# Optimization experiments

Hardware: AMD Instinct MI355X
Metric: run time of the kernel (lower is better)

The kernel has to match this reference:

```python
import jax, jax.numpy as jnp
import numpy as np

DIM, HEADS, B, S = 128, 4, 8, 80
BN_SCALE = np.float32(1.0 / np.sqrt(1.0 + 1e-5))  # eval-mode BatchNorm2d with running stats (0, 1)


def conv2d(x, w, b=None, groups=1, pad=0):
    y = jax.lax.conv_general_dilated(x, w, (1, 1), [(pad, pad), (pad, pad)],
                                     dimension_numbers=('NCHW', 'OIHW', 'NCHW'),
                                     feature_group_count=groups)
    return y if b is None else y + b[None, :, None, None]


def gate(x, w1, b1, g, bt, w2, b2):
    # Conv1x1 -> BatchNorm2d(eval) -> ReLU -> Conv1x1 -> Sigmoid
    y = conv2d(x, w1, b1)
    y = y * (g * BN_SCALE)[None, :, None, None] + bt[None, :, None, None]
    return jax.nn.sigmoid(conv2d(jax.nn.relu(y), w2, b2))


def layernorm(x, w, b):
    # Restormer WithBias LayerNorm over the channel dim
    mu = jnp.mean(x, 1, keepdims=True)
    var = jnp.var(x, 1, keepdims=True)
    return (x - mu) / jnp.sqrt(var + 1e-5) * w[None, :, None, None] + b[None, :, None, None]


def l2norm(x):
    # F.normalize(dim=-1) incl. complex: divide by L2 norm of |x|
    n = jnp.sqrt(jnp.sum(jnp.abs(x) ** 2, -1, keepdims=True))
    return x / jnp.maximum(n, 1e-12)


def split_heads(t):
    b, c, h, w = t.shape
    return t.reshape(b, HEADS, c // HEADS, h * w)


def _etb(x, ln1_w, ln1_b, ln2_w, ln2_b,
         f_temp, f_proj_w, f_w1, f_wb1, f_bn_g, f_bn_b, f_w2, f_wb2,
         s_temp, s_q1_w, s_q1_b, s_k1_w, s_k1_b, s_v1_w, s_v1_b,
         s_q3_w, s_q5_w, s_k3_w, s_k5_w, s_v3_w, s_v5_w, s_c3_w, s_c5_w, s_proj_w,
         ff_dw1_w, ff_dw2_w, ff_proj_w,
         ffg_w1, ffg_b1, ffg_bng, ffg_bnb, ffg_w2, ffg_b2,
         ffg1_w1, ffg1_b1, ffg1_bng, ffg1_bnb, ffg1_w2, ffg1_b2):
    b, c, h, w = x.shape
    G = c // 2
    xn = layernorm(x, ln1_w, ln1_b)
    # ---- Attention_F (the repeated fft2(x) calls in torch are identical; computed once) ----
    xf = jnp.fft.fft2(xn)
    qf = l2norm(split_heads(xf))  # q_f == k_f in the original code
    vf = split_heads(xf)
    attn = jnp.einsum('bhcn,bhdn->bhcd', qf, qf) * f_temp
    attn = jax.nn.softmax(attn.real, -1) + 1j * jax.nn.softmax(attn.imag, -1)
    # NOTE: torch applies ifft2 over the LAST TWO dims of [b, head, c, h*w] -> (c, h*w)
    out_f = jnp.abs(jnp.fft.ifft2(jnp.einsum('bhcd,bhdn->bhcn', attn, vf))).reshape(b, c, h, w)
    out_f_l = jnp.abs(jnp.fft.ifft2(gate(xf.real, f_w1, f_wb1, f_bn_g, f_bn_b, f_w2, f_wb2) * xf))
    a_f = conv2d(jnp.concatenate([out_f, out_f_l], 1), f_proj_w)
    # ---- Attention_S ----
    q1 = conv2d(xn, s_q1_w, s_q1_b)
    k1 = conv2d(xn, s_k1_w, s_k1_b)
    v1 = conv2d(xn, s_v1_w, s_v1_b)
    qs = jnp.concatenate([conv2d(q1, s_q3_w, groups=G, pad=1), conv2d(q1, s_q5_w, groups=G, pad=2)], 1)
    ks = jnp.concatenate([conv2d(k1, s_k3_w, groups=G, pad=1), conv2d(k1, s_k5_w, groups=G, pad=2)], 1)
    vs = jnp.concatenate([conv2d(v1, s_v3_w, groups=G, pad=1), conv2d(v1, s_v5_w, groups=G, pad=2)], 1)
    qn = l2norm(split_heads(qs))
    kn = l2norm(split_heads(ks))
    vh = split_heads(vs)
    attn_s = jax.nn.softmax(jnp.einsum('bhcn,bhdn->bhcd', qn, kn) * s_temp, -1)
    out_s = jnp.einsum('bhcd,bhdn->bhcn', attn_s, vh).reshape(b, c, h, w)
    out_s_l = jnp.concatenate([conv2d(xn, s_c3_w, groups=G, pad=1), conv2d(xn, s_c5_w, groups=G, pad=2)], 1)
    a_s = conv2d(jnp.concatenate([out_s, out_s_l], 1), s_proj_w)
    x = x + a_f + a_s
    # ---- FeedForward ----
    xn2 = layernorm(x, ln2_w, ln2_b)
    xf2 = jnp.fft.fft2(xn2)
    x_f = jnp.abs(gate(xf2.real, ffg_w1, ffg_b1, ffg_bng, ffg_bnb, ffg_w2, ffg_b2) * xf2)
    x_f_g = jax.nn.gelu(x_f, approximate=False) * x_f
    x_s = conv2d(xn2, ff_dw1_w, groups=c, pad=1)
    x_s_g = jax.nn.gelu(x_s, approximate=False) * x_s
    cat = jnp.concatenate([x_f_g, x_s_g], 1)  # [b, 2c, h, w]
    cf = jnp.fft.fft2(cat)
    x_f2b = jnp.abs(jnp.fft.ifft2(gate(cf.real, ffg1_w1, ffg1_b1, ffg1_bng, ffg1_bnb, ffg1_w2, ffg1_b2) * cf))
    x_s2b = conv2d(cat, ff_dw2_w, groups=c, pad=1)
    return x + conv2d(jnp.concatenate([x_f2b, x_s2b], 1), ff_proj_w)


def setup_inputs() -> dict:
    key = jax.random.key(0)
    ks = iter(jax.random.split(key, 64))
    rn = lambda shape, s=0.02: jax.random.normal(next(ks), shape, jnp.float32) * s
    d = {}
    d['x'] = jax.random.normal(next(ks), (B, DIM, S, S), jnp.float32)
    for n in ('ln1_w', 'ln2_w'):
        d[n] = jnp.ones((DIM,), jnp.float32)
    for n in ('ln1_b', 'ln2_b'):
        d[n] = jnp.zeros((DIM,), jnp.float32)
    d['f_temp'] = jnp.ones((HEADS, 1, 1), jnp.float32)
    d['s_temp'] = jnp.ones((HEADS, 1, 1), jnp.float32)
    d['f_proj_w'] = rn((DIM, 2 * DIM, 1, 1))
    d['s_proj_w'] = rn((DIM, 2 * DIM, 1, 1))
    r = DIM // 16
    d['f_w1'] = rn((r, DIM, 1, 1)); d['f_wb1'] = jnp.zeros((r,), jnp.float32)
    d['f_bn_g'] = jnp.ones((r,), jnp.float32); d['f_bn_b'] = jnp.zeros((r,), jnp.float32)
    d['f_w2'] = rn((DIM, r, 1, 1)); d['f_wb2'] = jnp.zeros((DIM,), jnp.float32)
    for n in ('s_q1', 's_k1', 's_v1'):
        d[n + '_w'] = rn((DIM, DIM, 1, 1)); d[n + '_b'] = jnp.zeros((DIM,), jnp.float32)
    for n in ('s_q3', 's_k3', 's_v3', 's_c3'):
        d[n + '_w'] = rn((DIM // 2, 2, 3, 3))
    for n in ('s_q5', 's_k5', 's_v5', 's_c5'):
        d[n + '_w'] = rn((DIM // 2, 2, 5, 5))
    d['ff_dw1_w'] = rn((DIM, 1, 3, 3))
    d['ff_dw2_w'] = rn((2 * DIM, 2, 3, 3))
    d['ff_proj_w'] = rn((DIM, 4 * DIM, 1, 1))
    d['ffg_w1'] = rn((r, DIM, 1, 1)); d['ffg_b1'] = jnp.zeros((r,), jnp.float32)
    d['ffg_bng'] = jnp.ones((r,), jnp.float32); d['ffg_bnb'] = jnp.zeros((r,), jnp.float32)
    d['ffg_w2'] = rn((DIM, r, 1, 1)); d['ffg_b2'] = jnp.zeros((DIM,), jnp.float32)
    d['ffg1_w1'] = rn((r, 2 * DIM, 1, 1)); d['ffg1_b1'] = jnp.zeros((r,), jnp.float32)
    d['ffg1_bng'] = jnp.ones((r,), jnp.float32); d['ffg1_bnb'] = jnp.zeros((r,), jnp.float32)
    d['ffg1_w2'] = rn((2 * DIM, r, 1, 1)); d['ffg1_b2'] = jnp.zeros((2 * DIM,), jnp.float32)
    return d


def reference(x, ln1_w, ln1_b, ln2_w, ln2_b,
              f_temp, f_proj_w, f_w1, f_wb1, f_bn_g, f_bn_b, f_w2, f_wb2,
              s_temp, s_q1_w, s_q1_b, s_k1_w, s_k1_b, s_v1_w, s_v1_b,
              s_q3_w, s_q5_w, s_k3_w, s_k5_w, s_v3_w, s_v5_w, s_c3_w, s_c5_w, s_proj_w,
              ff_dw1_w, ff_dw2_w, ff_proj_w,
              ffg_w1, ffg_b1, ffg_bng, ffg_bnb, ffg_w2, ffg_b2,
              ffg1_w1, ffg1_b1, ffg1_bng, ffg1_bnb, ffg1_w2, ffg1_b2):
    return _etb(x, ln1_w, ln1_b, ln2_w, ln2_b,
                f_temp, f_proj_w, f_w1, f_wb1, f_bn_g, f_bn_b, f_w2, f_wb2,
                s_temp, s_q1_w, s_q1_b, s_k1_w, s_k1_b, s_v1_w, s_v1_b,
                s_q3_w, s_q5_w, s_k3_w, s_k5_w, s_v3_w, s_v5_w, s_c3_w, s_c5_w, s_proj_w,
                ff_dw1_w, ff_dw2_w, ff_proj_w,
                ffg_w1, ffg_b1, ffg_bng, ffg_bnb, ffg_w2, ffg_b2,
                ffg1_w1, ffg1_b1, ffg1_bng, ffg1_bnb, ffg1_w2, ffg1_b2)
```

## Files before the change

kernel.cpp:

```cpp
#include <hip/hip_runtime.h>
#include <math.h>

#define DI __device__ __forceinline__

constexpr int B_ = 8, C_ = 128, H_ = 4, S_ = 80, N_ = 6400;
constexpr int P_ = B_ * N_;
constexpr int NSPL = 2;
constexpr float PI2 = 6.283185307179586f;
constexpr float BN_SC = 0.9999950000374997f;

typedef __attribute__((ext_vector_type(8))) short bf16x8;
typedef __attribute__((ext_vector_type(4))) float f32x4;

DI void cfma(float2& a, float2 u, float2 v) {
  a.x = fmaf(u.x, v.x, a.x); a.x = fmaf(-u.y, v.y, a.x);
  a.y = fmaf(u.x, v.y, a.y); a.y = fmaf(u.y, v.x, a.y);
}
DI float2 cmul(float2 u, float2 v) {
  return make_float2(u.x * v.x - u.y * v.y, u.x * v.y + u.y * v.x);
}
DI float gelu_mul(float m) {
  return 0.5f * m * (1.f + erff(m * 0.7071067811865476f)) * m;
}
DI unsigned short bf16_rn(float f) {
  union { float f; unsigned int u; } v; v.f = f;
  unsigned int u = v.u;
  return (unsigned short)((u + 0x7fffu + ((u >> 16) & 1u)) >> 16);
}

__global__ __launch_bounds__(256) void k_layernorm(const float* __restrict__ in,
    const float* __restrict__ w, const float* __restrict__ bb, float* __restrict__ out) {
  __shared__ float redS[4][64], redS2[4][64];
  __shared__ float muv[64], invv[64];
  const int tid = threadIdx.x;
  const int g = tid >> 6, l = tid & 63;
  const int p = blockIdx.x * 64 + l;
  const int b = p / N_, n = p % N_;
  const float* xp = in + (size_t)b * C_ * N_ + n;
  float s = 0.f, s2 = 0.f;
  for (int c = g * 32; c < g * 32 + 32; c++) {
    float v = xp[(size_t)c * N_];
    s += v; s2 = fmaf(v, v, s2);
  }
  redS[g][l] = s; redS2[g][l] = s2;
  __syncthreads();
  if (g == 0) {
    float ts  = redS[0][l] + redS[1][l] + redS[2][l] + redS[3][l];
    float ts2 = redS2[0][l] + redS2[1][l] + redS2[2][l] + redS2[3][l];
    float mu = ts * (1.f / C_);
    float var = ts2 * (1.f / C_) - mu * mu;
    muv[l] = mu; invv[l] = rsqrtf(var + 1e-5f);
  }
  __syncthreads();
  const float mu = muv[l], inv = invv[l];
  float* op = out + (size_t)b * C_ * N_ + n;
  for (int c = g * 32; c < g * 32 + 32; c++) {
    float v = xp[(size_t)c * N_];
    op[(size_t)c * N_] = (v - mu) * inv * w[c] + bb[c];
  }
}


__global__ __launch_bounds__(256) void k_fft2_r2c(const float* __restrict__ in, float2* __restrict__ out,
                                                  int nCh, int inCtot, int inCoff,
                                                  float2* __restrict__ out2, int inCoff2, int nimg,
                                                  float* __restrict__ nrm) {
  __shared__ float2 data[N_];
  __shared__ float2 tw[80];
  int img = blockIdx.x;
  float2* op;
  int coff;
  if (img >= nimg) { img -= nimg; op = out2 + (size_t)img * N_; coff = inCoff2; }
  else { op = out + (size_t)img * N_; coff = inCoff; }
  const int b = img / nCh, ch = img % nCh;
  const float* ip = in + ((size_t)b * inCtot + coff + ch) * N_;
  const int tid = threadIdx.x;
  float* dataR = (float*)data;
  if (tid < 80) { float a = -PI2 * (float)tid * (1.f / 80.f); float sv, cv; sincosf(a, &sv, &cv); tw[tid] = make_float2(cv, sv); }
  for (int i = tid; i < N_; i += 256) dataR[i] = ip[i];
  __syncthreads();
  const int rg = tid >> 4;
  const int kap = tid & 15;
  const int r0 = rg * 5;
  {
    float2 F[5][5];
    #pragma unroll
    for (int j = 0; j < 5; j++)
      #pragma unroll
      for (int q = 0; q < 5; q++) F[j][q] = make_float2(0.f, 0.f);
    int m16 = 0;
    for (int m = 0; m < 16; ++m) {
      float2 t = tw[5 * m16];
      #pragma unroll
      for (int j = 0; j < 5; j++) {
        const float* row = &dataR[(r0 + j) * 80 + 5 * m];
        #pragma unroll
        for (int q = 0; q < 5; q++) {
          float xv = row[q];
          F[j][q].x = fmaf(xv, t.x, F[j][q].x);
          F[j][q].y = fmaf(xv, t.y, F[j][q].y);
        }
      }
      m16 += kap; if (m16 >= 16) m16 -= 16;
    }
    __syncthreads();
    #pragma unroll
    for (int s = 0; s < 5; ++s) {
      const int k = kap + 16 * s;
      if (k <= 40) {
        float2 t1 = tw[k];
        float2 t2 = tw[(2 * k) % 80];
        float2 t3 = tw[(3 * k) % 80];
        float2 t4 = tw[(4 * k) % 80];
        #pragma unroll
        for (int j = 0; j < 5; j++) {
          float2 a = F[j][0];
          cfma(a, F[j][1], t1);
          cfma(a, F[j][2], t2);
          cfma(a, F[j][3], t3);
          cfma(a, F[j][4], t4);
          data[(r0 + j) * 80 + k] = a;
          if (k >= 1 && k <= 39) data[(r0 + j) * 80 + 80 - k] = make_float2(a.x, -a.y);
        }
      }
    }
  }
  __syncthreads();
  const int k0 = (tid & 15) * 5;
  const int kap2 = tid >> 4;
  float snrm = 0.f;
  {
    float2 G[5][5];
    #pragma unroll
    for (int q = 0; q < 5; q++)
      #pragma unroll
      for (int i = 0; i < 5; i++) G[q][i] = make_float2(0.f, 0.f);
    int m16 = 0;
    for (int m = 0; m < 16; ++m) {
      float2 t = tw[5 * m16];
      #pragma unroll
      for (int q = 0; q < 5; q++) {
        const float2* rowp = &data[(5 * m + q) * 80 + k0];
        #pragma unroll
        for (int i = 0; i < 5; i++) cfma(G[q][i], rowp[i], t);
      }
      m16 += kap2; if (m16 >= 16) m16 -= 16;
    }
    #pragma unroll
    for (int s = 0; s < 5; ++s) {
      const int k1 = kap2 + 16 * s;
      if (k1 <= 40) {
        float2 t1 = tw[k1];
        float2 t2 = tw[(2 * k1) % 80];
        float2 t3 = tw[(3 * k1) % 80];
        float2 t4 = tw[(4 * k1) % 80];
        const float wgt = (k1 == 0 || k1 == 40) ? 1.f : 2.f;
        #pragma unroll
        for (int i = 0; i < 5; i++) {
          float2 y = G[0][i];
          cfma(y, G[1][i], t1);
          cfma(y, G[2][i], t2);
          cfma(y, G[3][i], t3);
          cfma(y, G[4][i], t4);
          const int k2 = k0 + i;
          op[k1 * 80 + k2] = y;
          if (k1 >= 1 && k1 <= 39) {
            const int m2 = (k2 == 0) ? 0 : 80 - k2;
            op[(80 - k1) * 80 + m2] = make_float2(y.x, -y.y);
          }
          snrm += wgt * (y.x * y.x + y.y * y.y);
        }
      }
    }
  }
  if (nrm) {
    __syncthreads();
    float* red = (float*)data;
    red[tid] = snrm;
    __syncthreads();
    for (int st = 128; st > 0; st >>= 1) { if (tid < st) red[tid] += red[tid + st]; __syncthreads(); }
    if (tid == 0) nrm[img] = fmaxf(sqrtf(red[0]), 1e-12f);
  }
}

__global__ __launch_bounds__(256) void k_ifft2_abs(const float2* __restrict__ in, float* __restrict__ out,
                                                   int inC, int outCtot, int outCoff,
                                                   const float2* __restrict__ in2, int outCoff2, int nimg) {
  __shared__ float2 data[N_];
  __shared__ float2 tw[80];
  int img = blockIdx.x;
  const float2* ip;
  int coff;
  if (img >= nimg) { img -= nimg; ip = in2 + (size_t)img * N_; coff = outCoff2; }
  else { ip = in + (size_t)img * N_; coff = outCoff; }
  const int b = img / inC, ch = img % inC;
  float* op = out + ((size_t)b * outCtot + coff + ch) * N_;
  const int tid = threadIdx.x;
  if (tid < 80) { float a = PI2 * (float)tid * (1.f / 80.f); float sv, cv; sincosf(a, &sv, &cv); tw[tid] = make_float2(cv, sv); }
  for (int i = tid; i < N_; i += 256) data[i] = ip[i];
  __syncthreads();
  const int rg = tid >> 4;
  const int cg = tid & 15;
  float2 E[3][3], O[3][3];
  for (int j = 0; j < 3; j++)
    for (int i = 0; i < 3; i++) { E[j][i] = make_float2(0.f, 0.f); O[j][i] = make_float2(0.f, 0.f); }
  {
    int idx[3], inc[3];
    #pragma unroll
    for (int i = 0; i < 3; i++) { idx[i] = 0; inc[i] = (2 * (cg + 16 * i)) % 80; }
    for (int m = 0; m < 40; ++m) {
      float4 z[3]; float2 t[3];
      #pragma unroll
      for (int j = 0; j < 3; j++) z[j] = *(const float4*)&data[(rg + 16 * j) * 80 + 2 * m];
      #pragma unroll
      for (int i = 0; i < 3; i++) t[i] = tw[idx[i]];
      #pragma unroll
      for (int j = 0; j < 3; j++) {
        float2 ze = make_float2(z[j].x, z[j].y);
        float2 zo = make_float2(z[j].z, z[j].w);
        #pragma unroll
        for (int i = 0; i < 3; i++) { cfma(E[j][i], ze, t[i]); cfma(O[j][i], zo, t[i]); }
      }
      #pragma unroll
      for (int i = 0; i < 3; i++) { idx[i] += inc[i]; if (idx[i] >= 80) idx[i] -= 80; }
    }
  }
  __syncthreads();
  #pragma unroll
  for (int j = 0; j < 3; j++) {
    const int r = rg + 16 * j;
    if (r <= 40) {
      #pragma unroll
      for (int i = 0; i < 3; i++) {
        const int n2 = cg + 16 * i;
        if (n2 < 40) {
          float2 u = cmul(tw[n2], O[j][i]);
          data[r * 80 + n2]      = make_float2(E[j][i].x + u.x, E[j][i].y + u.y);
          data[r * 80 + n2 + 40] = make_float2(E[j][i].x - u.x, E[j][i].y - u.y);
        }
      }
    }
  }
  __syncthreads();
  const int r0 = (tid >> 4) * 5;
  const int k0 = (tid & 15) * 5;
  float accR[5][5];
  for (int j = 0; j < 5; j++)
    for (int i = 0; i < 5; i++) accR[j][i] = 0.f;
  {
    int idx[5];
    #pragma unroll
    for (int j = 0; j < 5; j++) idx[j] = r0 + j;
    for (int r = 1; r <= 39; ++r) {
      float2 d[5]; float2 t[5];
      #pragma unroll
      for (int i = 0; i < 5; i++) d[i] = data[r * 80 + k0 + i];
      #pragma unroll
      for (int j = 0; j < 5; j++) t[j] = tw[idx[j]];
      #pragma unroll
      for (int j = 0; j < 5; j++) {
        #pragma unroll
        for (int i = 0; i < 5; i++) {
          accR[j][i] = fmaf(t[j].x, d[i].x, accR[j][i]);
          accR[j][i] = fmaf(-t[j].y, d[i].y, accR[j][i]);
        }
      }
      #pragma unroll
      for (int j = 0; j < 5; j++) { idx[j] += r0 + j; if (idx[j] >= 80) idx[j] -= 80; }
    }
  }
  #pragma unroll
  for (int i = 0; i < 5; i++) {
    float2 b0 = data[k0 + i];
    float2 b40 = data[40 * 80 + k0 + i];
    #pragma unroll
    for (int j = 0; j < 5; j++) {
      float s40 = ((r0 + j) & 1) ? -b40.x : b40.x;
      float res = 2.f * accR[j][i] + b0.x + s40;
      op[(r0 + j) * 80 + k0 + i] = fabsf(res) * (1.f / (float)N_);
    }
  }
}

__global__ __launch_bounds__(256) void k_iff_combo(const float2* __restrict__ in6400, float* __restrict__ out6400,
                                                   const float2* __restrict__ inF, float* __restrict__ outF) {
  __shared__ float2 data[N_];
  __shared__ float2 tw[80];
  __shared__ float2 tws[80];
  const int tid = threadIdx.x;
  if (blockIdx.x < (unsigned)(B_ * C_)) {
    const int row = blockIdx.x;
    const float2* ip = in6400 + (size_t)row * N_;
    float* op = out6400 + (size_t)row * N_;
    if (tid < 80) {
      float a = PI2 * (float)tid * (1.f / 80.f); float sv, cv; sincosf(a, &sv, &cv); tw[tid] = make_float2(cv, sv);
      float a2 = PI2 * (float)tid * (1.f / 6400.f); sincosf(a2, &sv, &cv); tws[tid] = make_float2(cv, sv);
    }
    for (int i = tid; i < N_; i += 256) data[i] = ip[i];
    __syncthreads();
    {
      const int r0 = (tid >> 4) * 5;
      const int cg = tid & 15;
      float2 E[5][3], O[5][3];
      for (int j = 0; j < 5; j++)
        for (int i = 0; i < 3; i++) { E[j][i] = make_float2(0.f, 0.f); O[j][i] = make_float2(0.f, 0.f); }
      int idx[3], inc[3];
      #pragma unroll
      for (int i = 0; i < 3; i++) { idx[i] = 0; inc[i] = (2 * (cg + 16 * i)) % 80; }
      for (int m = 0; m < 40; ++m) {
        float2 xe[5], xo[5], t[3];
        #pragma unroll
        for (int j = 0; j < 5; j++) {
          xe[j] = data[(r0 + j) + 160 * m];
          xo[j] = data[(r0 + j) + 160 * m + 80];
        }
        #pragma unroll
        for (int i = 0; i < 3; i++) t[i] = tw[idx[i]];
        #pragma unroll
        for (int j = 0; j < 5; j++) {
          #pragma unroll
          for (int i = 0; i < 3; i++) { cfma(E[j][i], xe[j], t[i]); cfma(O[j][i], xo[j], t[i]); }
        }
        #pragma unroll
        for (int i = 0; i < 3; i++) { idx[i] += inc[i]; if (idx[i] >= 80) idx[i] -= 80; }
      }
      __syncthreads();
      #pragma unroll
      for (int j = 0; j < 5; j++) {
        const int k1 = r0 + j;
        #pragma unroll
        for (int i = 0; i < 3; i++) {
          const int n2 = cg + 16 * i;
          if (n2 < 40) {
            float2 u = cmul(tw[n2], O[j][i]);
            float2 Ap = make_float2(E[j][i].x + u.x, E[j][i].y + u.y);
            float2 Am = make_float2(E[j][i].x - u.x, E[j][i].y - u.y);
            int t6 = k1 * n2; int q = t6 / 80, s6 = t6 - q * 80;
            data[k1 * 80 + n2] = cmul(Ap, cmul(tw[q], tws[s6]));
            int t6b = k1 * (n2 + 40); int qb = t6b / 80, sb = t6b - qb * 80;
            data[k1 * 80 + n2 + 40] = cmul(Am, cmul(tw[qb], tws[sb]));
          }
        }
      }
    }
    __syncthreads();
    {
      const int rg5 = tid >> 3;
      const int cg5 = tid & 7;
      float2 E2[5][3], O2[5][3];
      for (int i = 0; i < 5; i++)
        for (int j = 0; j < 3; j++) { E2[i][j] = make_float2(0.f, 0.f); O2[i][j] = make_float2(0.f, 0.f); }
      int idx[5], inc[5];
      #pragma unroll
      for (int i = 0; i < 5; i++) { idx[i] = 0; inc[i] = (2 * (cg5 * 5 + i)) % 80; }
      int n2c[3];
      #pragma unroll
      for (int j = 0; j < 3; j++) { int n2 = rg5 + 32 * j; n2c[j] = (n2 < 80) ? n2 : 0; }
      for (int m = 0; m < 40; ++m) {
        float2 ae[3], ao[3], t[5];
        #pragma unroll
        for (int j = 0; j < 3; j++) {
          ae[j] = data[(2 * m) * 80 + n2c[j]];
          ao[j] = data[(2 * m + 1) * 80 + n2c[j]];
        }
        #pragma unroll
        for (int i = 0; i < 5; i++) t[i] = tw[idx[i]];
        #pragma unroll
        for (int i = 0; i < 5; i++) {
          #pragma unroll
          for (int j = 0; j < 3; j++) { cfma(E2[i][j], ae[j], t[i]); cfma(O2[i][j], ao[j], t[i]); }
        }
        #pragma unroll
        for (int i = 0; i < 5; i++) { idx[i] += inc[i]; if (idx[i] >= 80) idx[i] -= 80; }
      }
      #pragma unroll
      for (int i = 0; i < 5; i++) {
        const int n1 = cg5 * 5 + i;
        #pragma unroll
        for (int j = 0; j < 3; j++) {
          const int n2 = rg5 + 32 * j;
          if (n2 < 80) {
            float2 u = cmul(tw[n1], O2[i][j]);
            float2 o1 = make_float2(E2[i][j].x + u.x, E2[i][j].y + u.y);
            float2 o2 = make_float2(E2[i][j].x - u.x, E2[i][j].y - u.y);
            op[n1 * 80 + n2] = sqrtf(o1.x * o1.x + o1.y * o1.y) * (1.f / 6400.f);
            op[(n1 + 40) * 80 + n2] = sqrtf(o2.x * o2.x + o2.y * o2.y) * (1.f / 6400.f);
          }
        }
      }
    }
  } else {
    const int img = blockIdx.x - B_ * C_;
    const float2* ip = inF + (size_t)img * N_;
    float* op = outF + (size_t)img * N_;
    if (tid < 80) { float a = PI2 * (float)tid * (1.f / 80.f); float sv, cv; sincosf(a, &sv, &cv); tw[tid] = make_float2(cv, sv); }
    for (int i = tid; i < N_; i += 256) data[i] = ip[i];
    __syncthreads();
    const int rg = tid >> 4;
    const int cg = tid & 15;
    float2 E[3][3], O[3][3];
    for (int j = 0; j < 3; j++)
      for (int i = 0; i < 3; i++) { E[j][i] = make_float2(0.f, 0.f); O[j][i] = make_float2(0.f, 0.f); }
    {
      int idx[3], inc[3];
      #pragma unroll
      for (int i = 0; i < 3; i++) { idx[i] = 0; inc[i] = (2 * (cg + 16 * i)) % 80; }
      for (int m = 0; m < 40; ++m) {
        float4 z[3]; float2 t[3];
        #pragma unroll
        for (int j = 0; j < 3; j++) z[j] = *(const float4*)&data[(rg + 16 * j) * 80 + 2 * m];
        #pragma unroll
        for (int i = 0; i < 3; i++) t[i] = tw[idx[i]];
        #pragma unroll
        for (int j = 0; j < 3; j++) {
          float2 ze = make_float2(z[j].x, z[j].y);
          float2 zo = make_float2(z[j].z, z[j].w);
          #pragma unroll
          for (int i = 0; i < 3; i++) { cfma(E[j][i], ze, t[i]); cfma(O[j][i], zo, t[i]); }
        }
        #pragma unroll
        for (int i = 0; i < 3; i++) { idx[i] += inc[i]; if (idx[i] >= 80) idx[i] -= 80; }
      }
    }
    __syncthreads();
    #pragma unroll
    for (int j = 0; j < 3; j++) {
      const int r = rg + 16 * j;
      if (r <= 40) {
        #pragma unroll
        for (int i = 0; i < 3; i++) {
          const int n2 = cg + 16 * i;
          if (n2 < 40) {
            float2 u = cmul(tw[n2], O[j][i]);
            data[r * 80 + n2]      = make_float2(E[j][i].x + u.x, E[j][i].y + u.y);
            data[r * 80 + n2 + 40] = make_float2(E[j][i].x - u.x, E[j][i].y - u.y);
          }
        }
      }
    }
    __syncthreads();
    const int r0 = (tid >> 4) * 5;
    const int k0 = (tid & 15) * 5;
    float accR[5][5];
    for (int j = 0; j < 5; j++)
      for (int i = 0; i < 5; i++) accR[j][i] = 0.f;
    {
      int idx[5];
      #pragma unroll
      for (int j = 0; j < 5; j++) idx[j] = r0 + j;
      for (int r = 1; r <= 39; ++r) {
        float2 d[5]; float2 t[5];
        #pragma unroll
        for (int i = 0; i < 5; i++) d[i] = data[r * 80 + k0 + i];
        #pragma unroll
        for (int j = 0; j < 5; j++) t[j] = tw[idx[j]];
        #pragma unroll
        for (int j = 0; j < 5; j++) {
          #pragma unroll
          for (int i = 0; i < 5; i++) {
            accR[j][i] = fmaf(t[j].x, d[i].x, accR[j][i]);
            accR[j][i] = fmaf(-t[j].y, d[i].y, accR[j][i]);
          }
        }
        #pragma unroll
        for (int j = 0; j < 5; j++) { idx[j] += r0 + j; if (idx[j] >= 80) idx[j] -= 80; }
      }
    }
    #pragma unroll
    for (int i = 0; i < 5; i++) {
      float2 b0 = data[k0 + i];
      float2 b40 = data[40 * 80 + k0 + i];
      #pragma unroll
      for (int j = 0; j < 5; j++) {
        float s40 = ((r0 + j) & 1) ? -b40.x : b40.x;
        float res = 2.f * accR[j][i] + b0.x + s40;
        op[(r0 + j) * 80 + k0 + i] = fabsf(res) * (1.f / (float)N_);
      }
    }
  }
}

__global__ __launch_bounds__(256) void k_gateA(const float2* __restrict__ zA, const float2* __restrict__ zB,
    int split, int Cin, const float* __restrict__ W1, const float* __restrict__ b1,
    const float* __restrict__ g, const float* __restrict__ bt, float* __restrict__ hid) {
  __shared__ float w[8 * 256];
  __shared__ float red[4][64][9];
  const int tid = threadIdx.x;
  const int grp = tid >> 6, l = tid & 63;
  for (int i = tid; i < 8 * Cin; i += 256) w[i] = W1[i];
  __syncthreads();
  const int p = blockIdx.x * 64 + l;
  const int b = p / N_, n = p % N_;
  const int cpg = Cin / 4;
  float acc[8] = {0.f, 0.f, 0.f, 0.f, 0.f, 0.f, 0.f, 0.f};
  for (int ci = grp * cpg; ci < (grp + 1) * cpg; ci++) {
    const float2* src = (ci < split) ? (zA + ((size_t)b * split + ci) * N_ + n)
                                     : (zB + ((size_t)b * (Cin - split) + (ci - split)) * N_ + n);
    float v = src->x;
    #pragma unroll
    for (int j = 0; j < 8; j++) acc[j] = fmaf(w[j * Cin + ci], v, acc[j]);
  }
  #pragma unroll
  for (int j = 0; j < 8; j++) red[grp][l][j] = acc[j];
  __syncthreads();
  if (grp == 0) {
    #pragma unroll
    for (int j = 0; j < 8; j++) {
      float t = red[0][l][j] + red[1][l][j] + red[2][l][j] + red[3][l][j];
      float y = (t + b1[j]) * (g[j] * BN_SC) + bt[j];
      hid[((size_t)b * 8 + j) * N_ + n] = fmaxf(y, 0.f);
    }
  }
}

template <int MODE>
__global__ __launch_bounds__(256) void k_gateB(float2* __restrict__ zA, float2* __restrict__ zB,
    int split, int Cout, const float* __restrict__ W2, const float* __restrict__ b2,
    const float* __restrict__ hid, float* __restrict__ outR, int outCtot, int outCoff) {
  __shared__ float w[64 * 8];
  __shared__ float bb[64];
  const int tid = threadIdx.x;
  const int cobase = blockIdx.y * 64;
  for (int i = tid; i < 64 * 8; i += 256) w[i] = W2[cobase * 8 + i];
  for (int i = tid; i < 64; i += 256) bb[i] = b2[cobase + i];
  __syncthreads();
  const int p = blockIdx.x * 256 + tid;
  const int b = p / N_, n = p % N_;
  float h[8];
  #pragma unroll
  for (int j = 0; j < 8; j++) h[j] = hid[((size_t)b * 8 + j) * N_ + n];
  for (int co = 0; co < 64; co++) {
    const int gco = cobase + co;
    float t = bb[co];
    #pragma unroll
    for (int j = 0; j < 8; j++) t = fmaf(w[co * 8 + j], h[j], t);
    float sg = 1.f / (1.f + expf(-t));
    float2* zp = (gco < split) ? (zA + ((size_t)b * split + gco) * N_ + n)
                               : (zB + ((size_t)b * (Cout - split) + (gco - split)) * N_ + n);
    float2 z = *zp;
    if (MODE == 0) {
      zp->x = z.x * sg; zp->y = z.y * sg;
    } else {
      float m = sg * sqrtf(z.x * z.x + z.y * z.y);
      outR[((size_t)b * outCtot + outCoff + gco) * N_ + n] = gelu_mul(m);
    }
  }
}

__global__ __launch_bounds__(256) void k_conv1x1(const float* __restrict__ inA, const float* __restrict__ inB,
    int split, int Cin, int Cout, const float* __restrict__ W, const float* __restrict__ bias,
    const float* __restrict__ resid, float* __restrict__ out) {
  __shared__ unsigned int xlds[16][68];
  const int tid = threadIdx.x;
  const int lane = tid & 63, wv = tid >> 6;
  const int p0 = blockIdx.x * 64;
  const int b = p0 / N_, n0 = p0 % N_;
  const int laneco = lane & 15, lanek = lane >> 4;
  const int kA = lanek * 8;
  f32x4 acc[2][4];
  #pragma unroll
  for (int g = 0; g < 2; g++)
    #pragma unroll
    for (int f = 0; f < 4; f++) acc[g][f] = (f32x4){0.f, 0.f, 0.f, 0.f};
  for (int cb = 0; cb < Cin; cb += 32) {
    const float* src = (cb < split) ? (inA + ((size_t)b * split + cb) * N_)
                                    : (inB + ((size_t)b * (Cin - split) + (cb - split)) * N_);
    bf16x8 af[2];
    #pragma unroll
    for (int g = 0; g < 2; g++) {
      const float* wp = W + (size_t)(wv * 32 + g * 16 + laneco) * Cin + cb + kA;
      float4 w0 = *(const float4*)wp;
      float4 w1 = *(const float4*)(wp + 4);
      af[g][0] = (short)bf16_rn(w0.x); af[g][1] = (short)bf16_rn(w0.y);
      af[g][2] = (short)bf16_rn(w0.z); af[g][3] = (short)bf16_rn(w0.w);
      af[g][4] = (short)bf16_rn(w1.x); af[g][5] = (short)bf16_rn(w1.y);
      af[g][6] = (short)bf16_rn(w1.z); af[g][7] = (short)bf16_rn(w1.w);
    }
    __syncthreads();
    #pragma unroll
    for (int r = 0; r < 4; r++) {
      const int kb = wv * 4 + r;
      float e = src[(size_t)(2 * kb) * N_ + n0 + lane];
      float o = src[(size_t)(2 * kb + 1) * N_ + n0 + lane];
      xlds[kb][lane] = (unsigned int)bf16_rn(e) | ((unsigned int)bf16_rn(o) << 16);
    }
    __syncthreads();
    #pragma unroll
    for (int f = 0; f < 4; f++) {
      const int pos = f * 16 + laneco;
      const int kb0 = lanek * 4;
      union { bf16x8 v; unsigned int u[4]; } bu;
      bu.u[0] = xlds[kb0 + 0][pos];
      bu.u[1] = xlds[kb0 + 1][pos];
      bu.u[2] = xlds[kb0 + 2][pos];
      bu.u[3] = xlds[kb0 + 3][pos];
      #pragma unroll
      for (int g = 0; g < 2; g++)
        acc[g][f] = __builtin_amdgcn_mfma_f32_16x16x32_bf16(af[g], bu.v, acc[g][f], 0, 0, 0);
    }
  }
  #pragma unroll
  for (int g = 0; g < 2; g++) {
    #pragma unroll
    for (int f = 0; f < 4; f++) {
      #pragma unroll
      for (int r = 0; r < 4; r++) {
        const int co = wv * 32 + g * 16 + lanek * 4 + r;
        float v = acc[g][f][r];
        if (bias) v += bias[co];
        const size_t off = ((size_t)b * Cout + co) * N_ + n0 + f * 16 + laneco;
        if (resid) v += resid[off];
        out[off] = v;
      }
    }
  }
}

__global__ __launch_bounds__(256) void k_conv1x1_qkv(const float* __restrict__ in,
    const float* __restrict__ W0, const float* __restrict__ b0, float* __restrict__ o0,
    const float* __restrict__ W1, const float* __restrict__ b1, float* __restrict__ o1,
    const float* __restrict__ W2, const float* __restrict__ b2, float* __restrict__ o2) {
  __shared__ unsigned int xlds[16][68];
  const float* W    = (blockIdx.y == 0) ? W0 : (blockIdx.y == 1) ? W1 : W2;
  const float* bias = (blockIdx.y == 0) ? b0 : (blockIdx.y == 1) ? b1 : b2;
  float* out        = (blockIdx.y == 0) ? o0 : (blockIdx.y == 1) ? o1 : o2;
  const int tid = threadIdx.x;
  const int lane = tid & 63, wv = tid >> 6;
  const int p0 = blockIdx.x * 64;
  const int b = p0 / N_, n0 = p0 % N_;
  const int laneco = lane & 15, lanek = lane >> 4;
  const int kA = lanek * 8;
  f32x4 acc[2][4];
  #pragma unroll
  for (int g = 0; g < 2; g++)
    #pragma unroll
    for (int f = 0; f < 4; f++) acc[g][f] = (f32x4){0.f, 0.f, 0.f, 0.f};
  for (int cb = 0; cb < 128; cb += 32) {
    const float* src = in + ((size_t)b * 128 + cb) * N_;
    bf16x8 af[2];
    #pragma unroll
    for (int g = 0; g < 2; g++) {
      const float* wp = W + (size_t)(wv * 32 + g * 16 + laneco) * 128 + cb + kA;
      float4 w0 = *(const float4*)wp;
      float4 w1 = *(const float4*)(wp + 4);
      af[g][0] = (short)bf16_rn(w0.x); af[g][1] = (short)bf16_rn(w0.y);
      af[g][2] = (short)bf16_rn(w0.z); af[g][3] = (short)bf16_rn(w0.w);
      af[g][4] = (short)bf16_rn(w1.x); af[g][5] = (short)bf16_rn(w1.y);
      af[g][6] = (short)bf16_rn(w1.z); af[g][7] = (short)bf16_rn(w1.w);
    }
    __syncthreads();
    #pragma unroll
    for (int r = 0; r < 4; r++) {
      const int kb = wv * 4 + r;
      float e = src[(size_t)(2 * kb) * N_ + n0 + lane];
      float o = src[(size_t)(2 * kb + 1) * N_ + n0 + lane];
      xlds[kb][lane] = (unsigned int)bf16_rn(e) | ((unsigned int)bf16_rn(o) << 16);
    }
    __syncthreads();
    #pragma unroll
    for (int f = 0; f < 4; f++) {
      const int pos = f * 16 + laneco;
      const int kb0 = lanek * 4;
      union { bf16x8 v; unsigned int u[4]; } bu;
      bu.u[0] = xlds[kb0 + 0][pos];
      bu.u[1] = xlds[kb0 + 1][pos];
      bu.u[2] = xlds[kb0 + 2][pos];
      bu.u[3] = xlds[kb0 + 3][pos];
      #pragma unroll
      for (int g = 0; g < 2; g++)
        acc[g][f] = __builtin_amdgcn_mfma_f32_16x16x32_bf16(af[g], bu.v, acc[g][f], 0, 0, 0);
    }
  }
  #pragma unroll
  for (int g = 0; g < 2; g++) {
    #pragma unroll
    for (int f = 0; f < 4; f++) {
      #pragma unroll
      for (int r = 0; r < 4; r++) {
        const int co = wv * 32 + g * 16 + lanek * 4 + r;
        float v = acc[g][f][r] + bias[co];
        out[((size_t)b * 128 + co) * N_ + n0 + f * 16 + laneco] = v;
      }
    }
  }
}

__global__ __launch_bounds__(256) void k_gconv35_4(
    const float* __restrict__ inQ, const float* __restrict__ w3Q, const float* __restrict__ w5Q, float* __restrict__ outQ,
    const float* __restrict__ inK, const float* __restrict__ w3K, const float* __restrict__ w5K, float* __restrict__ outK,
    const float* __restrict__ inV, const float* __restrict__ w3V, const float* __restrict__ w5V, float* __restrict__ outV,
    const float* __restrict__ inC2, const float* __restrict__ w3C, const float* __restrict__ w5C, float* __restrict__ outC2) {
  __shared__ float tt[2][44][84];
  const float* in; const float* w3; const float* w5; float* out;
  if (blockIdx.y == 0)      { in = inQ;  w3 = w3Q; w5 = w5Q; out = outQ; }
  else if (blockIdx.y == 1) { in = inK;  w3 = w3K; w5 = w5K; out = outK; }
  else if (blockIdx.y == 2) { in = inV;  w3 = w3V; w5 = w5V; out = outV; }
  else                      { in = inC2; w3 = w3C; w5 = w5C; out = outC2; }
  const int blk = blockIdx.x;
  const int b = blk / 128;
  const int rem = blk % 128;
  const int o = rem >> 1, half = rem & 1;
  const int y0 = half * 40;
  const float* i0 = in + ((size_t)b * C_ + 2 * o) * N_;
  const int tid = threadIdx.x;
  for (int i = tid; i < 2 * 44 * 84; i += 256) {
    int ic = i / (44 * 84);
    int r = (i % (44 * 84)) / 84;
    int cc = i % 84;
    int gy = y0 + r - 2, gx = cc - 2;
    float v = 0.f;
    if (gy >= 0 && gy < 80 && gx >= 0 && gx < 80) v = i0[(size_t)ic * N_ + gy * 80 + gx];
    tt[ic][r][cc] = v;
  }
  float w3r[2][9], w5r[2][25];
  #pragma unroll
  for (int ic = 0; ic < 2; ic++) {
    #pragma unroll
    for (int k = 0; k < 9; k++) w3r[ic][k] = w3[(o * 2 + ic) * 9 + k];
    #pragma unroll
    for (int k = 0; k < 25; k++) w5r[ic][k] = w5[(o * 2 + ic) * 25 + k];
  }
  __syncthreads();
  for (int p = tid; p < 3200; p += 256) {
    const int ly = p / 80, x = p % 80;
    float a3 = 0.f, a5 = 0.f;
    #pragma unroll
    for (int ky = 0; ky < 5; ky++) {
      #pragma unroll
      for (int kx = 0; kx < 5; kx++) {
        float v0 = tt[0][ly + ky][x + kx];
        float v1 = tt[1][ly + ky][x + kx];
        a5 = fmaf(v0, w5r[0][ky * 5 + kx], a5);
        a5 = fmaf(v1, w5r[1][ky * 5 + kx], a5);
        if (ky >= 1 && ky < 4 && kx >= 1 && kx < 4) {
          int k3 = (ky - 1) * 3 + (kx - 1);
          a3 = fmaf(v0, w3r[0][k3], a3);
          a3 = fmaf(v1, w3r[1][k3], a3);
        }
// ... 389 lines not shown
```

Measured before the change: 1.041 ms.

## Replace radix-2 DFT split with 16x5 Cooley-Tukey decomposition in inverse FFT kernels

The 80-point DFT stages in the inverse FFT kernels move from an even/odd radix-2 split, with 40-length direct DFTs, to a 16x5 factorization. Each thread now computes 16-point partial sums over five interleaved subsequences and finishes with a radix-5 combine. The aim is to cut the complex FMA count per output and drop the conditional twiddle-index stepping. In exchange, per-thread register arrays get larger, shared-memory access patterns change, and the later stages must cover all 80 outputs directly instead of mirroring with ±.

Result: faster. 989.4 us (-5.0%).

```diff
diff --git a/kernel.cpp b/kernel.cpp
--- a/kernel.cpp
+++ b/kernel.cpp
@@ -199,44 +199,43 @@
   if (tid < 80) { float a = PI2 * (float)tid * (1.f / 80.f); float sv, cv; sincosf(a, &sv, &cv); tw[tid] = make_float2(cv, sv); }
   for (int i = tid; i < N_; i += 256) data[i] = ip[i];
   __syncthreads();
-  const int rg = tid >> 4;
-  const int cg = tid & 15;
-  float2 E[3][3], O[3][3];
-  for (int j = 0; j < 3; j++)
-    for (int i = 0; i < 3; i++) { E[j][i] = make_float2(0.f, 0.f); O[j][i] = make_float2(0.f, 0.f); }
   {
-    int idx[3], inc[3];
-    #pragma unroll
-    for (int i = 0; i < 3; i++) { idx[i] = 0; inc[i] = (2 * (cg + 16 * i)) % 80; }
-    for (int m = 0; m < 40; ++m) {
-      float4 z[3]; float2 t[3];
-      #pragma unroll
-      for (int j = 0; j < 3; j++) z[j] = *(const float4*)&data[(rg + 16 * j) * 80 + 2 * m];
-      #pragma unroll
-      for (int i = 0; i < 3; i++) t[i] = tw[idx[i]];
+    const int g1 = tid >> 4;
+    const int kap = tid & 15;
+    float2 F[3][5];
+    #pragma unroll
+    for (int j = 0; j < 3; j++)
+      #pragma unroll
+      for (int q = 0; q < 5; q++) F[j][q] = make_float2(0.f, 0.f);
+    int m16 = 0;
+    for (int m = 0; m < 16; ++m) {
+      float2 t = tw[5 * m16];
       #pragma unroll
       for (int j = 0; j < 3; j++) {
-        float2 ze = make_float2(z[j].x, z[j].y);
-        float2 zo = make_float2(z[j].z, z[j].w);
-        #pragma unroll
-        for (int i = 0; i < 3; i++) { cfma(E[j][i], ze, t[i]); cfma(O[j][i], zo, t[i]); }
-      }
-      #pragma unroll
-      for (int i = 0; i < 3; i++) { idx[i] += inc[i]; if (idx[i] >= 80) idx[i] -= 80; }
-    }
-  }
-  __syncthreads();
-  #pragma unroll
-  for (int j = 0; j < 3; j++) {
-    const int r = rg + 16 * j;
-    if (r <= 40) {
-      #pragma unroll
-      for (int i = 0; i < 3; i++) {
-        const int n2 = cg + 16 * i;
-        if (n2 < 40) {
-          float2 u = cmul(tw[n2], O[j][i]);
-          data[r * 80 + n2]      = make_float2(E[j][i].x + u.x, E[j][i].y + u.y);
-          data[r * 80 + n2 + 40] = make_float2(E[j][i].x - u.x, E[j][i].y - u.y);
+        const float2* rowp = &data[(g1 + 16 * j) * 80 + 5 * m];
+        #pragma unroll
+        for (int q = 0; q < 5; q++) cfma(F[j][q], rowp[q], t);
+      }
+      m16 += kap; if (m16 >= 16) m16 -= 16;
+    }
+    __syncthreads();
+    #pragma unroll
+    for (int s = 0; s < 5; ++s) {
+      const int n2 = kap + 16 * s;
+      float2 t1 = tw[n2];
+      float2 t2 = tw[(2 * n2) % 80];
+      float2 t3 = tw[(3 * n2) % 80];
+      float2 t4 = tw[(4 * n2) % 80];
+      #pragma unroll
+      for (int j = 0; j < 3; j++) {
+        const int r = g1 + 16 * j;
+        if (r <= 40) {
+          float2 a = F[j][0];
+          cfma(a, F[j][1], t1);
+          cfma(a, F[j][2], t2);
+          cfma(a, F[j][3], t3);
+          cfma(a, F[j][4], t4);
+          data[r * 80 + n2] = a;
         }
       }
     }
@@ -298,94 +297,80 @@
     }
     for (int i = tid; i < N_; i += 256) data[i] = ip[i];
     __syncthreads();
+    const int g = tid >> 4;
+    const int kap = tid & 15;
+    const int r0 = g * 5;
     {
-      const int r0 = (tid >> 4) * 5;
-      const int cg = tid & 15;
-      float2 E[5][3], O[5][3];
+      float2 F[5][5];
+      #pragma unroll
       for (int j = 0; j < 5; j++)
-        for (int i = 0; i < 3; i++) { E[j][i] = make_float2(0.f, 0.f); O[j][i] = make_float2(0.f, 0.f); }
-      int idx[3], inc[3];
-      #pragma unroll
-      for (int i = 0; i < 3; i++) { idx[i] = 0; inc[i] = (2 * (cg + 16 * i)) % 80; }
-      for (int m = 0; m < 40; ++m) {
-        float2 xe[5], xo[5], t[3];
+        #pragma unroll
+        for (int q = 0; q < 5; q++) F[j][q] = make_float2(0.f, 0.f);
+      int m16 = 0;
+      for (int m = 0; m < 16; ++m) {
+        float2 t = tw[5 * m16];
+        #pragma unroll
+        for (int q = 0; q < 5; q++) {
+          const float2* col = &data[(5 * m + q) * 80 + r0];
+          #pragma unroll
+          for (int j = 0; j < 5; j++) cfma(F[j][q], col[j], t);
+        }
+        m16 += kap; if (m16 >= 16) m16 -= 16;
+      }
+      __syncthreads();
+      #pragma unroll
+      for (int s = 0; s < 5; ++s) {
+        const int n2 = kap + 16 * s;
+        float2 t1 = tw[n2];
+        float2 t2 = tw[(2 * n2) % 80];
+        float2 t3 = tw[(3 * n2) % 80];
+        float2 t4 = tw[(4 * n2) % 80];
         #pragma unroll
         for (int j = 0; j < 5; j++) {
-          xe[j] = data[(r0 + j) + 160 * m];
-          xo[j] = data[(r0 + j) + 160 * m + 80];
-        }
-        #pragma unroll
-        for (int i = 0; i < 3; i++) t[i] = tw[idx[i]];
-        #pragma unroll
-        for (int j = 0; j < 5; j++) {
-          #pragma unroll
-          for (int i = 0; i < 3; i++) { cfma(E[j][i], xe[j], t[i]); cfma(O[j][i], xo[j], t[i]); }
-        }
-        #pragma unroll
-        for (int i = 0; i < 3; i++) { idx[i] += inc[i]; if (idx[i] >= 80) idx[i] -= 80; }
-      }
-      __syncthreads();
-      #pragma unroll
-      for (int j = 0; j < 5; j++) {
-        const int k1 = r0 + j;
-        #pragma unroll
-        for (int i = 0; i < 3; i++) {
-          const int n2 = cg + 16 * i;
-          if (n2 < 40) {
-            float2 u = cmul(tw[n2], O[j][i]);
-            float2 Ap = make_float2(E[j][i].x + u.x, E[j][i].y + u.y);
-            float2 Am = make_float2(E[j][i].x - u.x, E[j][i].y - u.y);
-            int t6 = k1 * n2; int q = t6 / 80, s6 = t6 - q * 80;
-            data[k1 * 80 + n2] = cmul(Ap, cmul(tw[q], tws[s6]));
-            int t6b = k1 * (n2 + 40); int qb = t6b / 80, sb = t6b - qb * 80;
-            data[k1 * 80 + n2 + 40] = cmul(Am, cmul(tw[qb], tws[sb]));
-          }
+          const int k1 = r0 + j;
+          float2 a = F[j][0];
+          cfma(a, F[j][1], t1);
+          cfma(a, F[j][2], t2);
+          cfma(a, F[j][3], t3);
+          cfma(a, F[j][4], t4);
+          int t6 = k1 * n2; int q6 = t6 / 80, s6 = t6 - q6 * 80;
+          data[k1 * 80 + n2] = cmul(a, cmul(tw[q6], tws[s6]));
         }
       }
     }
     __syncthreads();
     {
-      const int rg5 = tid >> 3;
-      const int cg5 = tid & 7;
-      float2 E2[5][3], O2[5][3];
-      for (int i = 0; i < 5; i++)
-        for (int j = 0; j < 3; j++) { E2[i][j] = make_float2(0.f, 0.f); O2[i][j] = make_float2(0.f, 0.f); }
-      int idx[5], inc[5];
-      #pragma unroll
-      for (int i = 0; i < 5; i++) { idx[i] = 0; inc[i] = (2 * (cg5 * 5 + i)) % 80; }
-      int n2c[3];
-      #pragma unroll
-      for (int j = 0; j < 3; j++) { int n2 = rg5 + 32 * j; n2c[j] = (n2 < 80) ? n2 : 0; }
-      for (int m = 0; m < 40; ++m) {
-        float2 ae[3], ao[3], t[5];
-        #pragma unroll
-        for (int j = 0; j < 3; j++) {
-          ae[j] = data[(2 * m) * 80 + n2c[j]];
-          ao[j] = data[(2 * m + 1) * 80 + n2c[j]];
-        }
-        #pragma unroll
-        for (int i = 0; i < 5; i++) t[i] = tw[idx[i]];
+      float2 G[5][5];
+      #pragma unroll
+      for (int q = 0; q < 5; q++)
+        #pragma unroll
+        for (int i = 0; i < 5; i++) G[q][i] = make_float2(0.f, 0.f);
+      int m16 = 0;
+      for (int m = 0; m < 16; ++m) {
+        float2 t = tw[5 * m16];
+        #pragma unroll
+        for (int q = 0; q < 5; q++) {
+          const float2* rowp = &data[(5 * m + q) * 80 + r0];
+          #pragma unroll
+          for (int i = 0; i < 5; i++) cfma(G[q][i], rowp[i], t);
+        }
+        m16 += kap; if (m16 >= 16) m16 -= 16;
+      }
+      #pragma unroll
+      for (int s = 0; s < 5; ++s) {
+        const int n1 = kap + 16 * s;
+        float2 t1 = tw[n1];
+        float2 t2 = tw[(2 * n1) % 80];
+        float2 t3 = tw[(3 * n1) % 80];
+        float2 t4 = tw[(4 * n1) % 80];
         #pragma unroll
         for (int i = 0; i < 5; i++) {
-          #pragma unroll
-          for (int j = 0; j < 3; j++) { cfma(E2[i][j], ae[j], t[i]); cfma(O2[i][j], ao[j], t[i]); }
-        }
-        #pragma unroll
-        for (int i = 0; i < 5; i++) { idx[i] += inc[i]; if (idx[i] >= 80) idx[i] -= 80; }
-      }
-      #pragma unroll
-      for (int i = 0; i < 5; i++) {
-        const int n1 = cg5 * 5 + i;
-        #pragma unroll
-        for (int j = 0; j < 3; j++) {
-          const int n2 = rg5 + 32 * j;
-          if (n2 < 80) {
-            float2 u = cmul(tw[n1], O2[i][j]);
-            float2 o1 = make_float2(E2[i][j].x + u.x, E2[i][j].y + u.y);
-            float2 o2 = make_float2(E2[i][j].x - u.x, E2[i][j].y - u.y);
-            op[n1 * 80 + n2] = sqrtf(o1.x * o1.x + o1.y * o1.y) * (1.f / 6400.f);
-            op[(n1 + 40) * 80 + n2] = sqrtf(o2.x * o2.x + o2.y * o2.y) * (1.f / 6400.f);
-          }
+          float2 y = G[0][i];
+          cfma(y, G[1][i], t1);
+          cfma(y, G[2][i], t2);
+          cfma(y, G[3][i], t3);
+          cfma(y, G[4][i], t4);
+          op[n1 * 80 + r0 + i] = sqrtf(y.x * y.x + y.y * y.y) * (1.f / 6400.f);
         }
       }
     }
@@ -396,44 +381,43 @@
     if (tid < 80) { float a = PI2 * (float)tid * (1.f / 80.f); float sv, cv; sincosf(a, &sv, &cv); tw[tid] = make_float2(cv, sv); }
     for (int i = tid; i < N_; i += 256) data[i] = ip[i];
     __syncthreads();
-    const int rg = tid >> 4;
-    const int cg = tid & 15;
-    float2 E[3][3], O[3][3];
-    for (int j = 0; j < 3; j++)
-      for (int i = 0; i < 3; i++) { E[j][i] = make_float2(0.f, 0.f); O[j][i] = make_float2(0.f, 0.f); }
     {
-      int idx[3], inc[3];
-      #pragma unroll
-      for (int i = 0; i < 3; i++) { idx[i] = 0; inc[i] = (2 * (cg + 16 * i)) % 80; }
-      for (int m = 0; m < 40; ++m) {
-        float4 z[3]; float2 t[3];
-        #pragma unroll
-        for (int j = 0; j < 3; j++) z[j] = *(const float4*)&data[(rg + 16 * j) * 80 + 2 * m];
-        #pragma unroll
-        for (int i = 0; i < 3; i++) t[i] = tw[idx[i]];
+      const int g1 = tid >> 4;
+      const int kap = tid & 15;
+      float2 F[3][5];
+      #pragma unroll
+      for (int j = 0; j < 3; j++)
+        #pragma unroll
+        for (int q = 0; q < 5; q++) F[j][q] = make_float2(0.f, 0.f);
+      int m16 = 0;
+      for (int m = 0; m < 16; ++m) {
+        float2 t = tw[5 * m16];
         #pragma unroll
         for (int j = 0; j < 3; j++) {
-          float2 ze = make_float2(z[j].x, z[j].y);
-          float2 zo = make_float2(z[j].z, z[j].w);
+          const float2* rowp = &data[(g1 + 16 * j) * 80 + 5 * m];
           #pragma unroll
-          for (int i = 0; i < 3; i++) { cfma(E[j][i], ze, t[i]); cfma(O[j][i], zo, t[i]); }
-        }
-        #pragma unroll
-        for (int i = 0; i < 3; i++) { idx[i] += inc[i]; if (idx[i] >= 80) idx[i] -= 80; }
-      }
-    }
-    __syncthreads();
-    #pragma unroll
-    for (int j = 0; j < 3; j++) {
-      const int r = rg + 16 * j;
-      if (r <= 40) {
-        #pragma unroll
-        for (int i = 0; i < 3; i++) {
-          const int n2 = cg + 16 * i;
-          if (n2 < 40) {
-            float2 u = cmul(tw[n2], O[j][i]);
-            data[r * 80 + n2]      = make_float2(E[j][i].x + u.x, E[j][i].y + u.y);
-            data[r * 80 + n2 + 40] = make_float2(E[j][i].x - u.x, E[j][i].y - u.y);
+          for (int q = 0; q < 5; q++) cfma(F[j][q], rowp[q], t);
+        }
+        m16 += kap; if (m16 >= 16) m16 -= 16;
+      }
+      __syncthreads();
+      #pragma unroll
+      for (int s = 0; s < 5; ++s) {
+        const int n2 = kap + 16 * s;
+        float2 t1 = tw[n2];
+        float2 t2 = tw[(2 * n2) % 80];
+        float2 t3 = tw[(3 * n2) % 80];
+        float2 t4 = tw[(4 * n2) % 80];
+        #pragma unroll
+        for (int j = 0; j < 3; j++) {
+          const int r = g1 + 16 * j;
+          if (r <= 40) {
+            float2 a = F[j][0];
+            cfma(a, F[j][1], t1);
+            cfma(a, F[j][2], t2);
+            cfma(a, F[j][3], t3);
+            cfma(a, F[j][4], t4);
+            data[r * 80 + n2] = a;
           }
         }
       }
```
